# Optimization experiments

Measured on AMD Instinct MI355X. Metric: run time of the kernel, lower is better.

Reference implementation:

```python
import jax, jax.numpy as jnp
import numpy as np

N = 50000   # nodes
E = 800000  # edges (avg degree 16)
D = 128     # hidden dim (GNN_hidden_dim), heads=1
SLOPE = 0.2  # LeakyReLU negative slope (PyG default)


def _w(k, shape, fan_in):
    return jax.random.normal(k, shape, dtype=jnp.float32) * (1.0 / np.sqrt(fan_in))


def setup_inputs() -> dict:
    key = jax.random.key(0)
    ks = jax.random.split(key, 24)
    inp = {}
    inp["x"] = jax.random.normal(ks[0], (N, D), dtype=jnp.float32)
    inp["edge_index"] = jax.random.randint(ks[1], (2, E), 0, N, dtype=jnp.int32)
    # layer 1 (GATv2 + linear skip)
    inp["Wl1"] = _w(ks[2], (D, D), D); inp["Wr1"] = _w(ks[3], (D, D), D)
    inp["att1"] = _w(ks[4], (D,), D); inp["b1"] = jnp.zeros((D,), jnp.float32)
    inp["Wlin1"] = _w(ks[5], (D, D), D); inp["blin1"] = jnp.zeros((D,), jnp.float32)
    # layer 2
    inp["Wl2"] = _w(ks[6], (D, D), D); inp["Wr2"] = _w(ks[7], (D, D), D)
    inp["att2"] = _w(ks[8], (D,), D); inp["b2"] = jnp.zeros((D,), jnp.float32)
    inp["Wlin2"] = _w(ks[9], (D, D), D); inp["blin2"] = jnp.zeros((D,), jnp.float32)
    # output layer (out_channels=1, heads=1)
    inp["Wlo"] = _w(ks[10], (D, 1), D); inp["Wro"] = _w(ks[11], (D, 1), D)
    inp["atto"] = _w(ks[12], (1,), 1); inp["bo"] = jnp.zeros((1,), jnp.float32)
    inp["Wlino"] = _w(ks[13], (D, 1), D); inp["blino"] = jnp.zeros((1,), jnp.float32)
    return inp


def gatv2(x, src, dst, Wl, Wr, att, b):
    # GATv2 (PyG, add_self_loops=False, share_weights=False, heads=1, no edge_attr)
    xl = x @ Wl            # [N, C] source transform (also message content)
    xr = x @ Wr            # [N, C] target transform
    e = jax.nn.leaky_relu(xl[src] + xr[dst], SLOPE) @ att  # [E] edge logits
    m = jax.ops.segment_max(e, dst, num_segments=N)
    m = jnp.where(jnp.isfinite(m), m, 0.0)  # empty segments
    p = jnp.exp(e - m[dst])
    s = jax.ops.segment_sum(p, dst, num_segments=N)
    alpha = p / (s[dst] + 1e-16)            # segment softmax over incoming edges
    out = jax.ops.segment_sum(alpha[:, None] * xl[src], dst, num_segments=N)
    return out + b


def reference(x, edge_index, Wl1, Wr1, att1, b1, Wlin1, blin1,
              Wl2, Wr2, att2, b2, Wlin2, blin2,
              Wlo, Wro, atto, bo, Wlino, blino):
    src, dst = edge_index[0], edge_index[1]
    h = jax.nn.relu(gatv2(x, src, dst, Wl1, Wr1, att1, b1) + x @ Wlin1 + blin1)
    h = jax.nn.relu(gatv2(h, src, dst, Wl2, Wr2, att2, b2) + h @ Wlin2 + blin2)
    out = gatv2(h, src, dst, Wlo, Wro, atto, bo) + h @ Wlino + blino
    return out  # [N, 1]
```

## Files before the change

### kernel.cpp

```cpp
#include <hip/hip_runtime.h>
#include <hip/hip_fp16.h>
#include <math.h>

#define NN 50000
#define EE 800000
#define DD 128
#define SLOPE 0.2f
#define NTILE 391

typedef __attribute__((ext_vector_type(8))) _Float16 half8;
typedef __attribute__((ext_vector_type(4))) float f32x4;

static __device__ __forceinline__ float wred_sum(float v) {
#pragma unroll
    for (int m = 1; m < 64; m <<= 1) v += __shfl_xor(v, m, 64);
    return v;
}

static __device__ __forceinline__ ushort f2h(float f) {
    __half h = __float2half(f);
    return *reinterpret_cast<ushort*>(&h);
}
static __device__ __forceinline__ __half2 u2h2(unsigned int u) {
    __half2 h;
    *reinterpret_cast<unsigned int*>(&h) = u;
    return h;
}
static __device__ __forceinline__ unsigned int h22u(__half2 h) {
    return *reinterpret_cast<unsigned int*>(&h);
}

__global__ void k_degree(const int* __restrict__ dstv, int* __restrict__ deg,
                         int* __restrict__ epos) {
    int i = blockIdx.x * blockDim.x + threadIdx.x;
    if (i < EE) epos[i] = atomicAdd(&deg[dstv[i]], 1);
}

__global__ void k_blocksum(const int* __restrict__ deg, int* __restrict__ bsum) {
    int t = threadIdx.x;
    int idx = blockIdx.x * 256 + t;
    int v = (idx < NN) ? deg[idx] : 0;
#pragma unroll
    for (int m = 1; m < 64; m <<= 1) v += __shfl_xor(v, m, 64);
    __shared__ int part[4];
    if ((t & 63) == 0) part[t >> 6] = v;
    __syncthreads();
    if (t == 0) bsum[blockIdx.x] = part[0] + part[1] + part[2] + part[3];
}

__global__ void k_scan_bsum(const int* __restrict__ bsum, int* __restrict__ boff, int nb) {
    __shared__ int sd[2][256];
    int t = threadIdx.x;
    int v = (t < nb) ? bsum[t] : 0;
    sd[0][t] = v;
    __syncthreads();
    int s = 0;
    for (int off = 1; off < 256; off <<= 1) {
        int x = sd[s][t];
        if (t >= off) x += sd[s][t - off];
        sd[s ^ 1][t] = x;
        s ^= 1;
        __syncthreads();
    }
    if (t < nb) boff[t] = sd[s][t] - v;
}

__global__ void k_scan_final(const int* __restrict__ deg, const int* __restrict__ boff,
                             int* __restrict__ offs) {
    __shared__ int sd[2][256];
    int t = threadIdx.x;
    int idx = blockIdx.x * 256 + t;
    int v = (idx < NN) ? deg[idx] : 0;
    sd[0][t] = v;
    __syncthreads();
    int s = 0;
    for (int off = 1; off < 256; off <<= 1) {
        int x = sd[s][t];
        if (t >= off) x += sd[s][t - off];
        sd[s ^ 1][t] = x;
        s ^= 1;
        __syncthreads();
    }
    int incl = sd[s][t];
    int base = boff[blockIdx.x];
    if (idx < NN) offs[idx + 1] = base + incl;
    if (idx == 0) offs[0] = 0;
}

__global__ void k_scatter(const int* __restrict__ srcv, const int* __restrict__ dstv,
                          const int* __restrict__ offs, const int* __restrict__ epos,
                          int* __restrict__ csr_src) {
    int i = blockIdx.x * blockDim.x + threadIdx.x;
    if (i < EE) csr_src[offs[dstv[i]] + epos[i]] = srcv[i];
}

__global__ __launch_bounds__(256) void k_wconvert(
    const float* __restrict__ W0, const float* __restrict__ W1, const float* __restrict__ W2,
    const float* __restrict__ W3, const float* __restrict__ W4, const float* __restrict__ W5,
    ushort* __restrict__ Wt) {
    int idx = blockIdx.x * 256 + threadIdx.x;
    int i = idx >> 14;
    int r = idx & 16383;
    int n = r >> 7;
    int k = r & 127;
    const float* Ws[6] = {W0, W1, W2, W3, W4, W5};
    Wt[idx] = f2h(Ws[i][k * DD + n]);
}

template <int XBF>
__global__ __launch_bounds__(256) void k_gemm3m(
    const float* __restrict__ Xf,
    const ushort* __restrict__ Xb,
    const ushort* __restrict__ Wt,
    ushort* __restrict__ O0b,
    ushort* __restrict__ O1b,
    ushort* __restrict__ O2b) {
    __shared__ ushort wsh[128 * 136];
    int t = threadIdx.x;
    int wid = t >> 6, lane = t & 63;
    int m0 = blockIdx.x * 128 + wid * 32;
    int qrow = lane & 15, kg = lane >> 4;

    half8 afrag[2][4];
#pragma unroll
    for (int mg = 0; mg < 2; mg++) {
#pragma unroll
        for (int ks = 0; ks < 4; ks++) {
            int row = m0 + mg * 16 + qrow;
            row = (row < NN) ? row : (NN - 1);
            if (XBF) {
                afrag[mg][ks] = *reinterpret_cast<const half8*>(
                    Xb + (size_t)row * DD + ks * 32 + kg * 8);
            } else {
                const float* p = Xf + (size_t)row * DD + ks * 32 + kg * 8;
                float4 u0 = *reinterpret_cast<const float4*>(p);
                float4 u1 = *reinterpret_cast<const float4*>(p + 4);
                half8 s;
                s[0] = (_Float16)u0.x; s[1] = (_Float16)u0.y;
                s[2] = (_Float16)u0.z; s[3] = (_Float16)u0.w;
                s[4] = (_Float16)u1.x; s[5] = (_Float16)u1.y;
                s[6] = (_Float16)u1.z; s[7] = (_Float16)u1.w;
                afrag[mg][ks] = s;
            }
        }
    }

    for (int w = 0; w < 3; w++) {
        __syncthreads();
        const ushort* Wb = Wt + (size_t)w * DD * DD;
#pragma unroll
        for (int i = 0; i < 8; i++) {
            int flat = i * 256 + t;
            int row = flat >> 4, ch = flat & 15;
            half8 v = *reinterpret_cast<const half8*>(Wb + row * DD + ch * 8);
            *reinterpret_cast<half8*>(&wsh[row * 136 + ch * 8]) = v;
        }
        __syncthreads();

        f32x4 acc[2][8];
#pragma unroll
        for (int mg = 0; mg < 2; mg++)
#pragma unroll
            for (int ng = 0; ng < 8; ng++) acc[mg][ng] = (f32x4)(0.f);

#pragma unroll
        for (int ks = 0; ks < 4; ks++) {
            half8 bfrag[8];
#pragma unroll
            for (int ng = 0; ng < 8; ng++)
                bfrag[ng] = *reinterpret_cast<const half8*>(
                    &wsh[(ng * 16 + qrow) * 136 + ks * 32 + kg * 8]);
#pragma unroll
            for (int mg = 0; mg < 2; mg++)
#pragma unroll
                for (int ng = 0; ng < 8; ng++)
                    acc[mg][ng] = __builtin_amdgcn_mfma_f32_16x16x32_f16(
                        afrag[mg][ks], bfrag[ng], acc[mg][ng], 0, 0, 0);
        }

        __syncthreads();
#pragma unroll
        for (int mg = 0; mg < 2; mg++) {
#pragma unroll
            for (int r = 0; r < 4; r++) {
                int lrow = wid * 32 + mg * 16 + kg * 4 + r;
#pragma unroll
                for (int ng = 0; ng < 8; ng++)
                    wsh[lrow * 136 + ng * 16 + qrow] = f2h(acc[mg][ng][r]);
            }
        }
        __syncthreads();
        ushort* Ob = (w == 0) ? O0b : (w == 1) ? O1b : O2b;
#pragma unroll
        for (int i = 0; i < 8; i++) {
            int flat = i * 64 + lane;
            int lrow = flat >> 4;
            int ch = flat & 15;
            int grow = m0 + lrow;
            if (grow < NN) {
                half8 v = *reinterpret_cast<const half8*>(
                    &wsh[(wid * 32 + lrow) * 136 + ch * 8]);
                *reinterpret_cast<half8*>(Ob + (size_t)grow * DD + ch * 8) = v;
            }
        }
    }
}

template <int OUTVEC>
__global__ __launch_bounds__(128) void k_fused(
    const int* __restrict__ offs, const int* __restrict__ csr_src,
    const ushort* __restrict__ xlb,
    const ushort* __restrict__ xrb,
    const float* __restrict__ att,
    const ushort* __restrict__ linb,
    const float* __restrict__ bb,
    const float* __restrict__ blin, ushort* __restrict__ houtb,
    const float* __restrict__ Wlo, const float* __restrict__ Wro,
    const float* __restrict__ Wlino, const float* __restrict__ blino,
    float* __restrict__ xlo, float* __restrict__ xro, float* __restrict__ lino) {
    int g = blockIdx.x + 8 * (blockIdx.y >> 6);
    if (g >= NTILE) return;
    int nb = g * 64 + (blockIdx.y & 63);
    int wid = nb * 2 + (threadIdx.x >> 6);
    if (wid >= NN) return;
    int lane = threadIdx.x & 63;
    int q = lane >> 4;
    int ql = lane & 15;
    int c0 = ql * 8;

    __half2 av6h[4], av4h[4];
    {
        float4 a0 = *reinterpret_cast<const float4*>(att + c0);
        float4 a1 = *reinterpret_cast<const float4*>(att + c0 + 4);
        float av[8] = {a0.x, a0.y, a0.z, a0.w, a1.x, a1.y, a1.z, a1.w};
#pragma unroll
        for (int c = 0; c < 4; c++) {
            av6h[c] = __halves2half2(__float2half(0.6f * av[2 * c]),
                                     __float2half(0.6f * av[2 * c + 1]));
            av4h[c] = __halves2half2(__float2half(0.4f * av[2 * c]),
                                     __float2half(0.4f * av[2 * c + 1]));
        }
    }
    __half2 xrv2[4];
    {
        uint4 xrp = *reinterpret_cast<const uint4*>(xrb + (size_t)wid * DD + c0);
        xrv2[0] = u2h2(xrp.x); xrv2[1] = u2h2(xrp.y);
        xrv2[2] = u2h2(xrp.z); xrv2[3] = u2h2(xrp.w);
    }

    int start = offs[wid];
    int deg = offs[wid + 1] - start;

    float ss = 0.f;
    __half2 acc2[4];
#pragma unroll
    for (int c = 0; c < 4; c++) acc2[c] = u2h2(0u);

    for (int eb = 0; eb < deg; eb += 64) {
        int nbv = min(64, deg - eb);
        int myidx = (lane < nbv) ? csr_src[start + eb + lane] : 0;
        int rounds = (nbv + 3) >> 2;
        int r = 0;
        for (; r + 2 <= rounds; r += 2) {
            int j0 = r * 4 + q;
            int j1 = j0 + 4;
            bool ok1 = j1 < nbv;
            int s0 = __shfl(myidx, j0, 64);
            int s1 = __shfl(myidx, j1, 64);
            uint4 xp0 = *reinterpret_cast<const uint4*>(xlb + (size_t)s0 * DD + c0);
            uint4 xp1 = *reinterpret_cast<const uint4*>(xlb + (size_t)s1 * DD + c0);
            __half2 xa[4] = {u2h2(xp0.x), u2h2(xp0.y), u2h2(xp0.z), u2h2(xp0.w)};
            __half2 xb[4] = {u2h2(xp1.x), u2h2(xp1.y), u2h2(xp1.z), u2h2(xp1.w)};
            __half2 va = u2h2(0u), vb = u2h2(0u);
#pragma unroll
            for (int c = 0; c < 4; c++) {
                __half2 ua = __hadd2(xa[c], xrv2[c]);
                __half2 ub = __hadd2(xb[c], xrv2[c]);
                __half2 aa = u2h2(h22u(ua) & 0x7fff7fffu);
                __half2 ab = u2h2(h22u(ub) & 0x7fff7fffu);
                va = __hfma2(ua, av6h[c], va);
                vb = __hfma2(ub, av6h[c], vb);
                va = __hfma2(aa, av4h[c], va);
                vb = __hfma2(ab, av4h[c], vb);
            }
            float v0 = __low2float(va) + __high2float(va);
            float v1 = __low2float(vb) + __high2float(vb);
#pragma unroll
            for (int msk = 1; msk < 16; msk <<= 1) {
                v0 += __shfl_xor(v0, msk, 64);
                v1 += __shfl_xor(v1, msk, 64);
            }
            float p0 = __expf(v0);
            float p1 = ok1 ? __expf(v1) : 0.f;
            ss += p0 + p1;
            __half2 p20 = __float2half2_rn(p0);
            __half2 p21 = __float2half2_rn(p1);
#pragma unroll
            for (int c = 0; c < 4; c++) {
                acc2[c] = __hfma2(p20, xa[c], acc2[c]);
                acc2[c] = __hfma2(p21, xb[c], acc2[c]);
            }
        }
        if (r < rounds) {
            int j = r * 4 + q;
            bool ok = j < nbv;
            int s = __shfl(myidx, j, 64);
            uint4 xp = *reinterpret_cast<const uint4*>(xlb + (size_t)s * DD + c0);
            __half2 xv2[4] = {u2h2(xp.x), u2h2(xp.y), u2h2(xp.z), u2h2(xp.w)};
            __half2 vs = u2h2(0u);
#pragma unroll
            for (int c = 0; c < 4; c++) {
                __half2 u2 = __hadd2(xv2[c], xrv2[c]);
                __half2 a2 = u2h2(h22u(u2) & 0x7fff7fffu);
                vs = __hfma2(u2, av6h[c], vs);
                vs = __hfma2(a2, av4h[c], vs);
            }
            float v = __low2float(vs) + __high2float(vs);
#pragma unroll
            for (int msk = 1; msk < 16; msk <<= 1) v += __shfl_xor(v, msk, 64);
            float p = ok ? __expf(v) : 0.f;
            ss += p;
            __half2 p2 = __float2half2_rn(p);
#pragma unroll
            for (int c = 0; c < 4; c++) acc2[c] = __hfma2(p2, xv2[c], acc2[c]);
        }
    }

#pragma unroll
    for (int msk = 16; msk < 64; msk <<= 1) {
        ss += __shfl_xor(ss, msk, 64);
#pragma unroll
        for (int c = 0; c < 4; c++) {
            unsigned int o = (unsigned int)__shfl_xor((int)h22u(acc2[c]), msk, 64);
            acc2[c] = __hadd2(acc2[c], u2h2(o));
        }
    }

    if (q == 0) {
        float inv = 1.f / (ss + 1e-16f);
        float o[8];
#pragma unroll
        for (int c = 0; c < 4; c++) {
            o[2 * c] = __low2float(acc2[c]) * inv;
            o[2 * c + 1] = __high2float(acc2[c]) * inv;
        }
        float lv[8];
        {
            uint4 lp = *reinterpret_cast<const uint4*>(linb + (size_t)wid * DD + c0);
            __half2 l2[4] = {u2h2(lp.x), u2h2(lp.y), u2h2(lp.z), u2h2(lp.w)};
#pragma unroll
            for (int c = 0; c < 4; c++) {
                lv[2 * c] = __low2float(l2[c]);
                lv[2 * c + 1] = __high2float(l2[c]);
            }
        }
        float4 b0 = *reinterpret_cast<const float4*>(bb + c0);
        float4 b1 = *reinterpret_cast<const float4*>(bb + c0 + 4);
        float4 bl0 = *reinterpret_cast<const float4*>(blin + c0);
        float4 bl1 = *reinterpret_cast<const float4*>(blin + c0 + 4);
        float bv[8] = {b0.x, b0.y, b0.z, b0.w, b1.x, b1.y, b1.z, b1.w};
        float blv[8] = {bl0.x, bl0.y, bl0.z, bl0.w, bl1.x, bl1.y, bl1.z, bl1.w};
#pragma unroll
        for (int c = 0; c < 8; c++) o[c] = fmaxf(o[c] + bv[c] + lv[c] + blv[c], 0.f);

        if (!OUTVEC) {
            uint4 pk;
            pk.x = (unsigned)f2h(o[0]) | ((unsigned)f2h(o[1]) << 16);
            pk.y = (unsigned)f2h(o[2]) | ((unsigned)f2h(o[3]) << 16);
            pk.z = (unsigned)f2h(o[4]) | ((unsigned)f2h(o[5]) << 16);
            pk.w = (unsigned)f2h(o[6]) | ((unsigned)f2h(o[7]) << 16);
            *reinterpret_cast<uint4*>(houtb + (size_t)wid * DD + c0) = pk;
        } else {
            float4 w0a = *reinterpret_cast<const float4*>(Wlo + c0);
            float4 w0b = *reinterpret_cast<const float4*>(Wlo + c0 + 4);
            float4 w1a = *reinterpret_cast<const float4*>(Wro + c0);
            float4 w1b = *reinterpret_cast<const float4*>(Wro + c0 + 4);
            float4 w2a = *reinterpret_cast<const float4*>(Wlino + c0);
            float4 w2b = *reinterpret_cast<const float4*>(Wlino + c0 + 4);
            float wv0[8] = {w0a.x, w0a.y, w0a.z, w0a.w, w0b.x, w0b.y, w0b.z, w0b.w};
            float wv1[8] = {w1a.x, w1a.y, w1a.z, w1a.w, w1b.x, w1b.y, w1b.z, w1b.w};
            float wv2[8] = {w2a.x, w2a.y, w2a.z, w2a.w, w2b.x, w2b.y, w2b.z, w2b.w};
            float d0 = 0.f, d1 = 0.f, d2 = 0.f;
#pragma unroll
            for (int c = 0; c < 8; c++) {
                d0 += o[c] * wv0[c];
                d1 += o[c] * wv1[c];
                d2 += o[c] * wv2[c];
            }
#pragma unroll
            for (int msk = 1; msk < 16; msk <<= 1) {
                d0 += __shfl_xor(d0, msk, 64);
                d1 += __shfl_xor(d1, msk, 64);
                d2 += __shfl_xor(d2, msk, 64);
            }
            if (ql == 0) {
                xlo[wid] = d0;
                xro[wid] = d1;
                lino[wid] = d2 + blino[0];
            }
        }
    }
}

__global__ __launch_bounds__(256) void k_aggout(
    const int* __restrict__ offs, const int* __restrict__ csr_src,
    const float* __restrict__ xlo, const float* __restrict__ xro,
    const float* __restrict__ atto, const float* __restrict__ lino,
    const float* __restrict__ bo, float* __restrict__ out) {
    int wid = (blockIdx.x * blockDim.x + threadIdx.x) >> 6;
    int lane = threadIdx.x & 63;
    if (wid >= NN) return;
    int start = offs[wid];
    int deg = offs[wid + 1] - start;
    float xro_w = xro[wid];
    float a0 = atto[0];

    float sl = 0.f, nl = 0.f;
    for (int j = lane; j < deg; j += 64) {
        int s = csr_src[start + j];
        float xs = xlo[s];
        float u = xs + xro_w;
        float e = fmaxf(u, SLOPE * u) * a0;
        float p = __expf(e);
        sl += p;
        nl += p * xs;
    }
    sl = wred_sum(sl);
    nl = wred_sum(nl);
    if (lane == 0) out[wid] = nl / (sl + 1e-16f) + bo[0] + lino[wid];
}

extern "C" void kernel_launch(void* const* d_in, const int* in_sizes, int n_in,
                              void* d_out, int out_size, void* d_ws, size_t ws_size,
                              hipStream_t stream) {
    const float* x = (const float*)d_in[0];
    const int* ei = (const int*)d_in[1];
    const int* srcv = ei;
    const int* dstv = ei + EE;
    const float* Wl1 = (const float*)d_in[2];
    const float* Wr1 = (const float*)d_in[3];
    const float* att1 = (const float*)d_in[4];
    const float* b1 = (const float*)d_in[5];
    const float* Wlin1 = (const float*)d_in[6];
    const float* blin1 = (const float*)d_in[7];
    const float* Wl2 = (const float*)d_in[8];
    const float* Wr2 = (const float*)d_in[9];
    const float* att2 = (const float*)d_in[10];
    const float* b2 = (const float*)d_in[11];
    const float* Wlin2 = (const float*)d_in[12];
    const float* blin2 = (const float*)d_in[13];
    const float* Wlo = (const float*)d_in[14];
    const float* Wro = (const float*)d_in[15];
    const float* atto = (const float*)d_in[16];
    const float* bo = (const float*)d_in[17];
    const float* Wlino = (const float*)d_in[18];
    const float* blino = (const float*)d_in[19];

    char* w = (char*)d_ws;
    auto alloc = [&](size_t bytes) {
        void* p = (void*)w;
        w += (bytes + 255) & ~(size_t)255;
        return p;
    };
    ushort* xlb = (ushort*)alloc((size_t)NN * DD * 2);
    ushort* xrb = (ushort*)alloc((size_t)NN * DD * 2);
    ushort* linb = (ushort*)alloc((size_t)NN * DD * 2);
    ushort* hb = (ushort*)alloc((size_t)NN * DD * 2);
    ushort* Wt = (ushort*)alloc((size_t)6 * DD * DD * 2);
    float* xlo = (float*)alloc((size_t)NN * 4);
    float* xro = (float*)alloc((size_t)NN * 4);
    float* lino = (float*)alloc((size_t)NN * 4);
    int* deg = (int*)alloc((size_t)NN * 4);
    int* offs = (int*)alloc((size_t)(NN + 1) * 4);
    int* bsum = (int*)alloc(256 * 4);
    int* boff = (int*)alloc(256 * 4);
    int* csr_src = (int*)alloc((size_t)(EE + 64) * 4);
    int* epos = (int*)alloc((size_t)EE * 4);

    const int NB = (NN + 255) / 256;

    hipMemsetAsync(deg, 0, (size_t)NN * 4, stream);
    k_degree<<<(EE + 255) / 256, 256, 0, stream>>>(dstv, deg, epos);
    k_blocksum<<<NB, 256, 0, stream>>>(deg, bsum);
    k_scan_bsum<<<1, 256, 0, stream>>>(bsum, boff, NB);
    k_scan_final<<<NB, 256, 0, stream>>>(deg, boff, offs);
    k_scatter<<<(EE + 255) / 256, 256, 0, stream>>>(srcv, dstv, offs, epos, csr_src);

    k_wconvert<<<(6 * DD * DD) / 256, 256, 0, stream>>>(Wl1, Wr1, Wlin1, Wl2, Wr2, Wlin2, Wt);

    const int GEMM_GRID = NTILE;
    const dim3 FUSED_GRID(8, 49 * 64);
    const int NODE_GRID = (NN * 64 + 255) / 256;

    k_gemm3m<0><<<GEMM_GRID, 256, 0, stream>>>(x, nullptr, Wt + (size_t)0 * 3 * DD * DD,
                                               xlb, xrb, linb);
    k_fused<0><<<FUSED_GRID, 128, 0, stream>>>(offs, csr_src, xlb, xrb, att1, linb, b1, blin1, hb,
                                               nullptr, nullptr, nullptr, nullptr,
                                               nullptr, nullptr, nullptr);
    k_gemm3m<1><<<GEMM_GRID, 256, 0, stream>>>(nullptr, hb, Wt + (size_t)1 * 3 * DD * DD,
                                               xlb, xrb, linb);
    k_fused<1><<<FUSED_GRID, 128, 0, stream>>>(offs, csr_src, xlb, xrb, att2, linb, b2, blin2,
                                               nullptr, Wlo, Wro, Wlino, blino,
                                               xlo, xro, lino);
    k_aggout<<<NODE_GRID, 256, 0, stream>>>(offs, csr_src, xlo, xro, atto, lino, bo, (float*)d_out);
}
```

Measured before the change: 188.9 us.

## Shrink GEMM tiles, linearize fused grid, 16-lane aggout groups, cursor-based CSR scatter

```diff
diff --git a/kernel.cpp b/kernel.cpp
--- a/kernel.cpp
+++ b/kernel.cpp
@@ -6,16 +6,9 @@
 #define EE 800000
 #define DD 128
 #define SLOPE 0.2f
-#define NTILE 391
 
 typedef __attribute__((ext_vector_type(8))) _Float16 half8;
 typedef __attribute__((ext_vector_type(4))) float f32x4;
-
-static __device__ __forceinline__ float wred_sum(float v) {
-#pragma unroll
-    for (int m = 1; m < 64; m <<= 1) v += __shfl_xor(v, m, 64);
-    return v;
-}
 
 static __device__ __forceinline__ ushort f2h(float f) {
     __half h = __float2half(f);
@@ -30,10 +23,9 @@
     return *reinterpret_cast<unsigned int*>(&h);
 }
 
-__global__ void k_degree(const int* __restrict__ dstv, int* __restrict__ deg,
-                         int* __restrict__ epos) {
+__global__ void k_degree(const int* __restrict__ dstv, int* __restrict__ deg) {
     int i = blockIdx.x * blockDim.x + threadIdx.x;
-    if (i < EE) epos[i] = atomicAdd(&deg[dstv[i]], 1);
+    if (i < EE) atomicAdd(&deg[dstv[i]], 1);
 }
 
 __global__ void k_blocksum(const int* __restrict__ deg, int* __restrict__ bsum) {
@@ -66,7 +58,7 @@
 }
 
 __global__ void k_scan_final(const int* __restrict__ deg, const int* __restrict__ boff,
-                             int* __restrict__ offs) {
+                             int* __restrict__ offs, int* __restrict__ cursor) {
     __shared__ int sd[2][256];
     int t = threadIdx.x;
     int idx = blockIdx.x * 256 + t;
@@ -83,15 +75,20 @@
     }
     int incl = sd[s][t];
     int base = boff[blockIdx.x];
-    if (idx < NN) offs[idx + 1] = base + incl;
+    if (idx < NN) {
+        offs[idx + 1] = base + incl;
+        cursor[idx] = base + incl - v;
+    }
     if (idx == 0) offs[0] = 0;
 }
 
 __global__ void k_scatter(const int* __restrict__ srcv, const int* __restrict__ dstv,
-                          const int* __restrict__ offs, const int* __restrict__ epos,
-                          int* __restrict__ csr_src) {
+                          int* __restrict__ cursor, int* __restrict__ csr_src) {
     int i = blockIdx.x * blockDim.x + threadIdx.x;
-    if (i < EE) csr_src[offs[dstv[i]] + epos[i]] = srcv[i];
+    if (i < EE) {
+        int p = atomicAdd(&cursor[dstv[i]], 1);
+        csr_src[p] = srcv[i];
+    }
 }
 
 __global__ __launch_bounds__(256) void k_wconvert(
@@ -118,18 +115,17 @@
     __shared__ ushort wsh[128 * 136];
     int t = threadIdx.x;
     int wid = t >> 6, lane = t & 63;
-    int m0 = blockIdx.x * 128 + wid * 32;
+    int m0 = blockIdx.x * 64 + wid * 16;
     int qrow = lane & 15, kg = lane >> 4;
 
-    half8 afrag[2][4];
-#pragma unroll
-    for (int mg = 0; mg < 2; mg++) {
+    half8 afrag[4];
+    {
+        int row = m0 + qrow;
+        row = (row < NN) ? row : (NN - 1);
 #pragma unroll
         for (int ks = 0; ks < 4; ks++) {
-            int row = m0 + mg * 16 + qrow;
-            row = (row < NN) ? row : (NN - 1);
             if (XBF) {
-                afrag[mg][ks] = *reinterpret_cast<const half8*>(
+                afrag[ks] = *reinterpret_cast<const half8*>(
                     Xb + (size_t)row * DD + ks * 32 + kg * 8);
             } else {
                 const float* p = Xf + (size_t)row * DD + ks * 32 + kg * 8;
@@ -140,7 +136,7 @@
                 s[2] = (_Float16)u0.z; s[3] = (_Float16)u0.w;
                 s[4] = (_Float16)u1.x; s[5] = (_Float16)u1.y;
                 s[6] = (_Float16)u1.z; s[7] = (_Float16)u1.w;
-                afrag[mg][ks] = s;
+                afrag[ks] = s;
             }
         }
     }
@@ -157,49 +153,40 @@
         }
         __syncthreads();
 
-        f32x4 acc[2][8];
-#pragma unroll
-        for (int mg = 0; mg < 2; mg++)
-#pragma unroll
-            for (int ng = 0; ng < 8; ng++) acc[mg][ng] = (f32x4)(0.f);
+        f32x4 acc[8];
+#pragma unroll
+        for (int ng = 0; ng < 8; ng++) acc[ng] = (f32x4)(0.f);
 
 #pragma unroll
         for (int ks = 0; ks < 4; ks++) {
-            half8 bfrag[8];
+#pragma unroll
+            for (int ng = 0; ng < 8; ng++) {
+                half8 bfrag = *reinterpret_cast<const half8*>(
+                    &wsh[(ng * 16 + qrow) * 136 + ks * 32 + kg * 8]);
+                acc[ng] = __builtin_amdgcn_mfma_f32_16x16x32_f16(
+                    afrag[ks], bfrag, acc[ng], 0, 0, 0);
+            }
+        }
+
+        __syncthreads();
+#pragma unroll
+        for (int r = 0; r < 4; r++) {
+            int lrow = wid * 16 + kg * 4 + r;
 #pragma unroll
             for (int ng = 0; ng < 8; ng++)
-                bfrag[ng] = *reinterpret_cast<const half8*>(
-                    &wsh[(ng * 16 + qrow) * 136 + ks * 32 + kg * 8]);
-#pragma unroll
-            for (int mg = 0; mg < 2; mg++)
-#pragma unroll
-                for (int ng = 0; ng < 8; ng++)
-                    acc[mg][ng] = __builtin_amdgcn_mfma_f32_16x16x32_f16(
-                        afrag[mg][ks], bfrag[ng], acc[mg][ng], 0, 0, 0);
-        }
-
-        __syncthreads();
-#pragma unroll
-        for (int mg = 0; mg < 2; mg++) {
-#pragma unroll
-            for (int r = 0; r < 4; r++) {
-                int lrow = wid * 32 + mg * 16 + kg * 4 + r;
-#pragma unroll
-                for (int ng = 0; ng < 8; ng++)
-                    wsh[lrow * 136 + ng * 16 + qrow] = f2h(acc[mg][ng][r]);
-            }
+                wsh[lrow * 136 + ng * 16 + qrow] = f2h(acc[ng][r]);
         }
         __syncthreads();
         ushort* Ob = (w == 0) ? O0b : (w == 1) ? O1b : O2b;
 #pragma unroll
-        for (int i = 0; i < 8; i++) {
+        for (int i = 0; i < 4; i++) {
             int flat = i * 64 + lane;
             int lrow = flat >> 4;
             int ch = flat & 15;
             int grow = m0 + lrow;
             if (grow < NN) {
                 half8 v = *reinterpret_cast<const half8*>(
-                    &wsh[(wid * 32 + lrow) * 136 + ch * 8]);
+                    &wsh[(wid * 16 + lrow) * 136 + ch * 8]);
                 *reinterpret_cast<half8*>(Ob + (size_t)grow * DD + ch * 8) = v;
             }
         }
@@ -218,10 +205,7 @@
     const float* __restrict__ Wlo, const float* __restrict__ Wro,
     const float* __restrict__ Wlino, const float* __restrict__ blino,
     float* __restrict__ xlo, float* __restrict__ xro, float* __restrict__ lino) {
-    int g = blockIdx.x + 8 * (blockIdx.y >> 6);
-    if (g >= NTILE) return;
-    int nb = g * 64 + (blockIdx.y & 63);
-    int wid = nb * 2 + (threadIdx.x >> 6);
+    int wid = blockIdx.x * 2 + (threadIdx.x >> 6);
     if (wid >= NN) return;
     int lane = threadIdx.x & 63;
     int q = lane >> 4;
@@ -407,8 +391,10 @@
     const float* __restrict__ xlo, const float* __restrict__ xro,
     const float* __restrict__ atto, const float* __restrict__ lino,
     const float* __restrict__ bo, float* __restrict__ out) {
-    int wid = (blockIdx.x * blockDim.x + threadIdx.x) >> 6;
     int lane = threadIdx.x & 63;
+    int g = lane >> 4;
+    int gl = lane & 15;
+    int wid = (blockIdx.x * blockDim.x + threadIdx.x) / 64 * 4 + g;
     if (wid >= NN) return;
     int start = offs[wid];
     int deg = offs[wid + 1] - start;
@@ -416,7 +402,7 @@
     float a0 = atto[0];
 
     float sl = 0.f, nl = 0.f;
-    for (int j = lane; j < deg; j += 64) {
+    for (int j = gl; j < deg; j += 16) {
         int s = csr_src[start + j];
         float xs = xlo[s];
         float u = xs + xro_w;
@@ -425,9 +411,12 @@
         sl += p;
         nl += p * xs;
     }
-    sl = wred_sum(sl);
-    nl = wred_sum(nl);
-    if (lane == 0) out[wid] = nl / (sl + 1e-16f) + bo[0] + lino[wid];
+#pragma unroll
+    for (int msk = 1; msk < 16; msk <<= 1) {
+        sl += __shfl_xor(sl, msk, 64);
+        nl += __shfl_xor(nl, msk, 64);
+    }
+    if (gl == 0) out[wid] = nl / (sl + 1e-16f) + bo[0] + lino[wid];
 }
 
 extern "C" void kernel_launch(void* const* d_in, const int* in_sizes, int n_in,
@@ -472,25 +461,25 @@
     float* lino = (float*)alloc((size_t)NN * 4);
     int* deg = (int*)alloc((size_t)NN * 4);
     int* offs = (int*)alloc((size_t)(NN + 1) * 4);
+    int* cursor = (int*)alloc((size_t)NN * 4);
     int* bsum = (int*)alloc(256 * 4);
     int* boff = (int*)alloc(256 * 4);
     int* csr_src = (int*)alloc((size_t)(EE + 64) * 4);
-    int* epos = (int*)alloc((size_t)EE * 4);
 
     const int NB = (NN + 255) / 256;
 
     hipMemsetAsync(deg, 0, (size_t)NN * 4, stream);
-    k_degree<<<(EE + 255) / 256, 256, 0, stream>>>(dstv, deg, epos);
+    k_degree<<<(EE + 255) / 256, 256, 0, stream>>>(dstv, deg);
     k_blocksum<<<NB, 256, 0, stream>>>(deg, bsum);
     k_scan_bsum<<<1, 256, 0, stream>>>(bsum, boff, NB);
-    k_scan_final<<<NB, 256, 0, stream>>>(deg, boff, offs);
-    k_scatter<<<(EE + 255) / 256, 256, 0, stream>>>(srcv, dstv, offs, epos, csr_src);
+    k_scan_final<<<NB, 256, 0, stream>>>(deg, boff, offs, cursor);
+    k_scatter<<<(EE + 255) / 256, 256, 0, stream>>>(srcv, dstv, cursor, csr_src);
 
     k_wconvert<<<(6 * DD * DD) / 256, 256, 0, stream>>>(Wl1, Wr1, Wlin1, Wl2, Wr2, Wlin2, Wt);
 
-    const int GEMM_GRID = NTILE;
-    const dim3 FUSED_GRID(8, 49 * 64);
-    const int NODE_GRID = (NN * 64 + 255) / 256;
+    const int GEMM_GRID = (NN + 63) / 64;
+    const int FUSED_GRID = (NN + 1) / 2;
+    const int AGGOUT_GRID = (NN + 15) / 16;
 
     k_gemm3m<0><<<GEMM_GRID, 256, 0, stream>>>(x, nullptr, Wt + (size_t)0 * 3 * DD * DD,
                                                xlb, xrb, linb);
@@ -502,5 +491,6 @@
     k_fused<1><<<FUSED_GRID, 128, 0, stream>>>(offs, csr_src, xlb, xrb, att2, linb, b2, blin2,
                                                nullptr, Wlo, Wro, Wlino, blino,
                                                xlo, xro, lino);
-    k_aggout<<<NODE_GRID, 256, 0, stream>>>(offs, csr_src, xlo, xro, atto, lino, bo, (float*)d_out);
-}
+    k_aggout<<<AGGOUT_GRID, 256, 0, stream>>>(offs, csr_src, xlo, xro, atto, lino, bo,
+                                              (float*)d_out);
+}
```

New measurement: 222.6 us. 17.8% more time.
